# Optimization experiments

Hardware: AMD Instinct MI355X
Metric: run time of the kernel (lower is better)

Reference implementation:

```python
import jax, jax.numpy as jnp
import numpy as np

L, D, H, HK, DH, F, V, T, B = 8, 1024, 16, 4, 64, 2816, 32000, 1024, 2
G = H // HK
THETA = 10000.0
EPS = 1e-6
SCALE = DH ** -0.5


def _rope_tables(t, dh, theta):
    inv = 1.0 / theta ** (jnp.arange(0, dh, 2, dtype=jnp.float32) / dh)  # [dh/2]
    ang = jnp.arange(t, dtype=jnp.float32)[:, None] * inv[None, :]       # [T, dh/2]
    return jnp.cos(ang), jnp.sin(ang)


def _apply_rope(x, cos, sin):
    # x: [B, T, h, DH] -> rotate pairs (even, odd)
    xr = x.reshape(*x.shape[:-1], DH // 2, 2)
    x0, x1 = xr[..., 0], xr[..., 1]
    c = cos[None, :, None, :]
    s = sin[None, :, None, :]
    out = jnp.stack([x0 * c - x1 * s, x0 * s + x1 * c], axis=-1)
    return out.reshape(*x.shape)


def _rmsnorm(x, w):
    var = jnp.mean(x * x, axis=-1, keepdims=True)
    return x * jax.lax.rsqrt(var + EPS) * w


def setup_inputs() -> dict:
    key = jax.random.key(0)
    ks = jax.random.split(key, 10)
    s = 0.02
    return {
        "ids": jax.random.randint(ks[0], (B, T), 0, V),
        "emb": jax.random.normal(ks[1], (V, D), jnp.float32) * s,
        "qw": jax.random.normal(ks[2], (L, H * DH, D), jnp.float32) * s,
        "kw": jax.random.normal(ks[3], (L, HK * DH, D), jnp.float32) * s,
        "vw": jax.random.normal(ks[4], (L, HK * DH, D), jnp.float32) * s,
        "ow": jax.random.normal(ks[5], (L, D, D), jnp.float32) * s,
        "w1": jax.random.normal(ks[6], (L, F, D), jnp.float32) * s,
        "w2": jax.random.normal(ks[7], (L, D, F), jnp.float32) * s,
        "w3": jax.random.normal(ks[8], (L, F, D), jnp.float32) * s,
        "n1": jnp.ones((L, D), jnp.float32),
        "n2": jnp.ones((L, D), jnp.float32),
        "nf": jnp.ones((D,), jnp.float32),
    }


def _forward(ids, emb, qw, kw, vw, ow, w1, w2, w3, n1, n2, nf):
    cos, sin = _rope_tables(T, DH, THETA)
    causal = jnp.tril(jnp.ones((T, T), dtype=bool))  # [T, T]
    x = emb[ids]  # [B, T, D]
    for l in range(L):
        xn = _rmsnorm(x, n1[l])
        q = jnp.einsum("btd,ed->bte", xn, qw[l]).reshape(B, T, H, DH)
        k = jnp.einsum("btd,ed->bte", xn, kw[l]).reshape(B, T, HK, DH)
        v = jnp.einsum("btd,ed->bte", xn, vw[l]).reshape(B, T, HK, DH)
        q = _apply_rope(q, cos, sin)
        k = _apply_rope(k, cos, sin)
        # GQA: group query heads over shared kv heads
        qg = q.transpose(0, 2, 1, 3).reshape(B, HK, G, T, DH)
        kh = k.transpose(0, 2, 1, 3)  # [B, HK, T, DH]
        vh = v.transpose(0, 2, 1, 3)
        scores = jnp.einsum("bkgtd,bksd->bkgts", qg, kh) * SCALE
        scores = jnp.where(causal, scores, -jnp.inf)
        p = jax.nn.softmax(scores, axis=-1)
        out = jnp.einsum("bkgts,bksd->bkgtd", p, vh)
        out = out.reshape(B, H, T, DH).transpose(0, 2, 1, 3).reshape(B, T, D)
        x = x + jnp.einsum("btd,ed->bte", out, ow[l])
        xn2 = _rmsnorm(x, n2[l])
        h1 = jnp.einsum("btd,fd->btf", xn2, w1[l])
        h3 = jnp.einsum("btd,fd->btf", xn2, w3[l])
        x = x + jnp.einsum("btf,df->btd", jax.nn.silu(h1) * h3, w2[l])
    x = _rmsnorm(x, nf)
    logits = jnp.einsum("btd,vd->btv", x, emb)  # tied lm_head
    return logits


def reference(ids, emb, qw, kw, vw, ow, w1, w2, w3, n1, n2, nf):
    return _forward(ids, emb, qw, kw, vw, ow, w1, w2, w3, n1, n2, nf)
```

## Files before the change

kernel.cpp:

```cpp
#include <hip/hip_runtime.h>
#include <math.h>

#define L_ 8
#define D_ 1024
#define H_ 16
#define HK_ 4
#define DH_ 64
#define F_ 2816
#define V_ 32000
#define T_ 1024
#define B_ 2
#define M_ (B_*T_)
#define SCALE_ 0.125f

typedef unsigned short u16;
typedef unsigned int   u32;
typedef __attribute__((ext_vector_type(4))) float  f32x4;
typedef __attribute__((ext_vector_type(8))) short  bf16x8;
typedef __attribute__((ext_vector_type(4))) unsigned short u16x4;
typedef __attribute__((ext_vector_type(4))) unsigned int   u32x4;

__device__ __forceinline__ float bf2f(u16 h) {
    union { u32 u; float f; } v; v.u = ((u32)h) << 16; return v.f;
}
__device__ __forceinline__ u16 f2bf(float f) {
    union { float f; u32 u; } v; v.f = f;
    u32 r = v.u + 0x7fffu + ((v.u >> 16) & 1u);
    return (u16)(r >> 16);
}

__device__ __forceinline__ void gl_lds16(const void* g, void* l) {
    __builtin_amdgcn_global_load_lds(
        (const __attribute__((address_space(1))) unsigned int*)g,
        (__attribute__((address_space(3))) unsigned int*)l,
        16, 0, 0);
}

template<int BM, int EPI>
__global__ __launch_bounds__(256)
void gemm2_k(const u16* __restrict__ A, int K,
             const u16* __restrict__ W, int N,
             float* __restrict__ Of, u16* __restrict__ Ob)
{
    constexpr int FM = BM / 32;
    constexpr int FN = 4;
    constexpr int GM = M_ / BM;
    constexpr int IPA = BM / 64;
    __shared__ u16 sA[2 * BM * 32];
    __shared__ u16 sB[2 * 128 * 32];

    const int tid  = threadIdx.x;
    const int lane = tid & 63, wv = tid >> 6;
    const int wm = wv >> 1, wn = wv & 1;
    const int l15 = lane & 15, lhi = lane >> 4;
    const int m0 = wm * (BM / 2), n0 = wn * 64;

    const int nwg = gridDim.x;
    const int q8 = nwg >> 3, r8 = nwg & 7;
    const int xcd = blockIdx.x & 7, off8 = blockIdx.x >> 3;
    const int wgid = (xcd < r8 ? xcd * (q8 + 1) : r8 * (q8 + 1) + (xcd - r8) * q8) + off8;
    const int tM = wgid % GM, tN = wgid / GM;

    const int srow = lane >> 2;
    const int scol = (lane & 3) * 8;

    const u16* Abase = A + (size_t)(tM * BM) * K;
    const u16* Wbase = W + (size_t)(tN * 128) * K;

    f32x4 acc[FM][FN];
#pragma unroll
    for (int i = 0; i < FM; ++i)
#pragma unroll
        for (int j = 0; j < FN; ++j) acc[i][j] = f32x4{0.f, 0.f, 0.f, 0.f};

    auto stage = [&](int kt, int buf) {
        u16* sa = sA + buf * (BM * 32);
        u16* sb = sB + buf * (128 * 32);
#pragma unroll
        for (int i = 0; i < IPA; ++i) {
            int c = wv * IPA + i;
            gl_lds16(Abase + (size_t)(c * 16 + srow) * K + kt + scol, sa + c * 512);
        }
#pragma unroll
        for (int i = 0; i < 2; ++i) {
            int c = wv * 2 + i;
            gl_lds16(Wbase + (size_t)(c * 16 + srow) * K + kt + scol, sb + c * 512);
        }
    };

    const int nt = K >> 5;
    stage(0, 0);
    asm volatile("s_waitcnt vmcnt(0)" ::: "memory");
    __syncthreads();

    int cur = 0;
    for (int t = 0; t < nt; ++t) {
        if (t + 1 < nt) stage((t + 1) << 5, cur ^ 1);

        const u16* sa = sA + cur * (BM * 32);
        const u16* sb = sB + cur * (128 * 32);
        bf16x8 av[FM], bv[FN];
#pragma unroll
        for (int i = 0; i < FM; ++i)
            av[i] = *(const bf16x8*)&sa[(m0 + i * 16 + l15) * 32 + lhi * 8];
#pragma unroll
        for (int j = 0; j < FN; ++j)
            bv[j] = *(const bf16x8*)&sb[(n0 + j * 16 + l15) * 32 + lhi * 8];
#pragma unroll
        for (int i = 0; i < FM; ++i)
#pragma unroll
            for (int j = 0; j < FN; ++j)
                acc[i][j] = __builtin_amdgcn_mfma_f32_16x16x32_bf16(
                    av[i], bv[j], acc[i][j], 0, 0, 0);

        if (t + 1 < nt) {
            asm volatile("s_waitcnt vmcnt(0)" ::: "memory");
            __syncthreads();
            cur ^= 1;
        }
    }

#pragma unroll
    for (int i = 0; i < FM; ++i)
#pragma unroll
        for (int j = 0; j < FN; ++j) {
            size_t gm = (size_t)tM * BM + m0 + i * 16 + lhi * 4;
            size_t gn = (size_t)tN * 128 + n0 + j * 16 + l15;
#pragma unroll
            for (int r = 0; r < 4; ++r) {
                float v = acc[i][j][r];
                size_t idx = (gm + r) * (size_t)N + gn;
                if (EPI == 0)      Ob[idx] = f2bf(v);
                else if (EPI == 1) Of[idx] = v;
                else               Of[idx] += v;
            }
        }
}

__global__ __launch_bounds__(256)
void cvt_k(const float* __restrict__ src, u16* __restrict__ dst,
           unsigned long long sStride, unsigned long long dStride)
{
    int l = blockIdx.y;
    size_t i = ((size_t)blockIdx.x * 256 + threadIdx.x) * 4;
    f32x4 v = *(const f32x4*)(src + l * sStride + i);
    u16x4 o;
    o.x = f2bf(v.x); o.y = f2bf(v.y); o.z = f2bf(v.z); o.w = f2bf(v.w);
    *(u16x4*)(dst + l * dStride + i) = o;
}

template<int BM, int BN, int EPI, int NW>
__global__ __launch_bounds__(256)
void gemm_k(const u16* __restrict__ A, int K,
            const float* __restrict__ W0, const float* __restrict__ W1p,
            const float* __restrict__ W2p, int N0, int N1, int N,
            float* __restrict__ Of, u16* __restrict__ Ob)
{
    constexpr int FM = BM / 32;
    constexpr int FN = BN / 32;
    constexpr int LS = 40;
    __shared__ u16 sA[BM * LS];
    __shared__ u16 sB[BN * LS];

    const int tid  = threadIdx.x;
    const int lane = tid & 63, wv = tid >> 6;
    const int wm = wv >> 1, wn = wv & 1;
    const int l15 = lane & 15, lhi = lane >> 4;
    const int m0 = wm * (BM / 2), n0 = wn * (BN / 2);
    const int tM = blockIdx.y, tN = blockIdx.x;

    f32x4 acc[FM][FN];
#pragma unroll
    for (int i = 0; i < FM; ++i)
#pragma unroll
        for (int j = 0; j < FN; ++j) acc[i][j] = f32x4{0.f, 0.f, 0.f, 0.f};

    for (int kt = 0; kt < K; kt += 32) {
#pragma unroll
        for (int i = 0; i < BM / 64; ++i) {
            int cid = tid + i * 256;
            int row = cid >> 2, kc = cid & 3;
            const u16* src = A + (size_t)(tM * BM + row) * K + kt + kc * 8;
            *(u32x4*)&sA[row * LS + kc * 8] = *(const u32x4*)src;
        }
#pragma unroll
        for (int i = 0; i < BN / 32; ++i) {
            int cid = tid + i * 256;
            int row = cid >> 3, kc = cid & 7;
            int n = tN * BN + row;
            const float* wr;
            if (NW == 1)      wr = W0 + (size_t)n * K;
            else if (NW == 2) wr = (n < N0) ? (W0 + (size_t)n * K)
                                            : (W1p + (size_t)(n - N0) * K);
            else              wr = (n < N0) ? (W0 + (size_t)n * K)
                               : (n < N0 + N1) ? (W1p + (size_t)(n - N0) * K)
                                               : (W2p + (size_t)(n - N0 - N1) * K);
            f32x4 v = *(const f32x4*)(wr + kt + kc * 4);
            u16x4 o;
            o.x = f2bf(v.x); o.y = f2bf(v.y); o.z = f2bf(v.z); o.w = f2bf(v.w);
            *(u16x4*)&sB[row * LS + kc * 4] = o;
        }
        __syncthreads();

        bf16x8 av[FM], bv[FN];
#pragma unroll
        for (int i = 0; i < FM; ++i)
            av[i] = *(const bf16x8*)&sA[(m0 + i * 16 + l15) * LS + lhi * 8];
#pragma unroll
        for (int j = 0; j < FN; ++j)
            bv[j] = *(const bf16x8*)&sB[(n0 + j * 16 + l15) * LS + lhi * 8];
#pragma unroll
        for (int i = 0; i < FM; ++i)
#pragma unroll
            for (int j = 0; j < FN; ++j)
                acc[i][j] = __builtin_amdgcn_mfma_f32_16x16x32_bf16(
                    av[i], bv[j], acc[i][j], 0, 0, 0);
        __syncthreads();
    }

#pragma unroll
    for (int i = 0; i < FM; ++i)
#pragma unroll
        for (int j = 0; j < FN; ++j) {
            size_t gm = (size_t)tM * BM + m0 + i * 16 + lhi * 4;
            size_t gn = (size_t)tN * BN + n0 + j * 16 + l15;
#pragma unroll
            for (int r = 0; r < 4; ++r) {
                float v = acc[i][j][r];
                size_t idx = (gm + r) * (size_t)N + gn;
                if (EPI == 0)      Ob[idx] = f2bf(v);
                else if (EPI == 1) Of[idx] = v;
                else               Of[idx] += v;
            }
        }
}

__global__ __launch_bounds__(256)
void vtrans_k(const u16* __restrict__ qkv, u16* __restrict__ vt)
{
    int rr = blockIdx.x;
    int d = rr & 63, hk = (rr >> 6) & 3, b = rr >> 8;
    int t = threadIdx.x * 4;
    const u16* base = qkv + (size_t)(b * T_ + t) * 1536 + 1280 + hk * 64 + d;
    u16 a0 = base[0];
    u16 a1 = base[1536];
    u16 a2 = base[3072];
    u16 a3 = base[4608];
    u16x4 o; o.x = a0; o.y = a1; o.z = a2; o.w = a3;
    *(u16x4*)(vt + (size_t)rr * T_ + t) = o;
}

__global__ __launch_bounds__(256)
void attn2_k(const u16* __restrict__ qkv, const u16* __restrict__ vt,
             u16* __restrict__ attn)
{
    const int qt = blockIdx.x, h = blockIdx.y, b = blockIdx.z;
    const int hk = h >> 2;
    const int tid = threadIdx.x;
    const int lane = tid & 63, w = tid >> 6;
    const int l15 = lane & 15, lhi = lane >> 4;

    __shared__ u16 sK[128 * 64];
    __shared__ u16 sVT[64 * 128];
    __shared__ u16 sP[4][16 * 136];

    const int q0 = qt * 64;
    const u16* qptr = qkv + (size_t)(b * T_ + q0 + w * 16 + l15) * 1536 + h * 64 + lhi * 8;
    bf16x8 aq0 = *(const bf16x8*)qptr;
    bf16x8 aq1 = *(const bf16x8*)(qptr + 32);

    f32x4 accO[4];
#pragma unroll
    for (int d = 0; d < 4; ++d) accO[d] = f32x4{0.f, 0.f, 0.f, 0.f};
    float m_r[4] = {-1e30f, -1e30f, -1e30f, -1e30f};
    float l_r[4] = {0.f, 0.f, 0.f, 0.f};
    const int myq = q0 + w * 16 + lhi * 4;
    const int qmaxw = q0 + w * 16 + 15;
    u16* sPw = sP[w];

    const int ntiles = (qt + 2) >> 1;
    const u16* vtb = vt + (size_t)((b * HK_ + hk) * DH_) * T_;
    const int L = lane;

    for (int kt = 0; kt < ntiles; ++kt) {
        const int t0 = kt * 128;
#pragma unroll
        for (int i = 0; i < 4; ++i) {
            int c = w * 4 + i;
            int row = c * 8 + (L >> 3);
            int p = L & 7;
            const u16* src = qkv + (size_t)(b * T_ + t0 + row) * 1536 + 1024 + hk * 64
                             + ((p ^ (row & 7)) * 8);
            gl_lds16(src, sK + c * 512);
        }
#pragma unroll
        for (int i = 0; i < 4; ++i) {
            int c = w * 4 + i;
            int row = c * 4 + (L >> 4);
            int p = L & 15;
            const u16* src = vtb + (size_t)row * T_ + t0 + ((p ^ (row & 15)) * 8);
            gl_lds16(src, sVT + c * 512);
        }
        asm volatile("s_waitcnt vmcnt(0)" ::: "memory");
        __syncthreads();

        const bool lastt = (kt == ntiles - 1);

        f32x4 accS[8];
#pragma unroll
        for (int nf = 0; nf < 8; ++nf)
            accS[nf] = f32x4{-1e30f, -1e30f, -1e30f, -1e30f};
#pragma unroll
        for (int pk = 0; pk < 4; ++pk) {
            if (t0 + pk * 32 > qmaxw) continue;
            f32x4 s0 = f32x4{0.f, 0.f, 0.f, 0.f};
            f32x4 s1 = f32x4{0.f, 0.f, 0.f, 0.f};
#pragma unroll
            for (int kk = 0; kk < 2; ++kk) {
                bf16x8 aqs = kk ? aq1 : aq0;
                int r0 = (pk * 2) * 16 + l15;
                int r1 = (pk * 2 + 1) * 16 + l15;
                int ls = kk * 4 + lhi;
                bf16x8 b0 = *(const bf16x8*)&sK[r0 * 64 + ((ls ^ (r0 & 7)) * 8)];
                bf16x8 b1 = *(const bf16x8*)&sK[r1 * 64 + ((ls ^ (r1 & 7)) * 8)];
                s0 = __builtin_amdgcn_mfma_f32_16x16x32_bf16(aqs, b0, s0, 0, 0, 0);
                s1 = __builtin_amdgcn_mfma_f32_16x16x32_bf16(aqs, b1, s1, 0, 0, 0);
            }
#pragma unroll
            for (int r = 0; r < 4; ++r) {
                float v0 = s0[r] * SCALE_;
                float v1 = s1[r] * SCALE_;
                if (lastt) {
                    int kp0 = t0 + (pk * 2) * 16 + l15;
                    int kp1 = kp0 + 16;
                    if (kp0 > myq + r) v0 = -1e30f;
                    if (kp1 > myq + r) v1 = -1e30f;
                }
                accS[pk * 2][r] = v0;
                accS[pk * 2 + 1][r] = v1;
            }
        }

        float sc[4];
#pragma unroll
        for (int r = 0; r < 4; ++r) {
            float mx = accS[0][r];
#pragma unroll
            for (int nf = 1; nf < 8; ++nf) mx = fmaxf(mx, accS[nf][r]);
#pragma unroll
            for (int off = 1; off < 16; off <<= 1) mx = fmaxf(mx, __shfl_xor(mx, off));
            float mn = fmaxf(m_r[r], mx);
            sc[r] = expf(m_r[r] - mn);
            m_r[r] = mn;
        }
        float rs[4] = {0.f, 0.f, 0.f, 0.f};
#pragma unroll
        for (int pk = 0; pk < 4; ++pk) {
            if (t0 + pk * 32 > qmaxw) continue;
#pragma unroll
            for (int g = 0; g < 2; ++g) {
                int nf = pk * 2 + g;
#pragma unroll
                for (int r = 0; r < 4; ++r) {
                    float p = expf(accS[nf][r] - m_r[r]);
                    accS[nf][r] = p;
                    rs[r] += p;
                }
            }
        }
#pragma unroll
        for (int r = 0; r < 4; ++r) {
#pragma unroll
            for (int off = 1; off < 16; off <<= 1) rs[r] += __shfl_xor(rs[r], off);
            l_r[r] = l_r[r] * sc[r] + rs[r];
        }
#pragma unroll
        for (int d = 0; d < 4; ++d)
#pragma unroll
            for (int r = 0; r < 4; ++r) accO[d][r] *= sc[r];

#pragma unroll
        for (int pk = 0; pk < 4; ++pk) {
            if (t0 + pk * 32 > qmaxw) continue;
#pragma unroll
            for (int g = 0; g < 2; ++g) {
                int nf = pk * 2 + g;
#pragma unroll
                for (int r = 0; r < 4; ++r)
                    sPw[(lhi * 4 + r) * 136 + nf * 16 + l15] = f2bf(accS[nf][r]);
            }
        }

#pragma unroll
        for (int kk = 0; kk < 4; ++kk) {
            if (t0 + kk * 32 > qmaxw) continue;
            bf16x8 pas = *(const bf16x8*)&sPw[l15 * 136 + kk * 32 + lhi * 8];
#pragma unroll
            for (int nf = 0; nf < 4; ++nf) {
                int row = nf * 16 + l15;
                int ls = kk * 4 + lhi;
                bf16x8 bvv = *(const bf16x8*)&sVT[row * 128 + ((ls ^ (row & 15)) * 8)];
                accO[nf] = __builtin_amdgcn_mfma_f32_16x16x32_bf16(pas, bvv, accO[nf], 0, 0, 0);
            }
        }
        __syncthreads();
    }

#pragma unroll
    for (int d = 0; d < 4; ++d)
#pragma unroll
        for (int r = 0; r < 4; ++r) {
            int row = q0 + w * 16 + lhi * 4 + r;
            float o = accO[d][r] / l_r[r];
            attn[(size_t)(b * T_ + row) * 1024 + h * 64 + d * 16 + l15] = f2bf(o);
        }
}

__global__ __launch_bounds__(256)
void attn_k(const u16* __restrict__ qkv, u16* __restrict__ attn)
{
    const int qt = blockIdx.x, h = blockIdx.y, b = blockIdx.z;
    const int hk = h >> 2;
    const int tid = threadIdx.x;
    const int lane = tid & 63, w = tid >> 6;
    const int l15 = lane & 15, lhi = lane >> 4;
    __shared__ u16 sK[64 * 72];
    __shared__ u16 sVT[64 * 74];
    __shared__ u16 sP[4 * 16 * 72];

    const int q0 = qt * 64;
    const u16* qptr = qkv + (size_t)(b * T_ + q0 + w * 16 + l15) * 1536 + h * 64 + lhi * 8;
    bf16x8 aq0 = *(const bf16x8*)qptr;
    bf16x8 aq1 = *(const bf16x8*)(qptr + 32);

    f32x4 accO[4];
#pragma unroll
    for (int d = 0; d < 4; ++d) accO[d] = f32x4{0.f, 0.f, 0.f, 0.f};
    float m_r[4] = {-1e30f, -1e30f, -1e30f, -1e30f};
    float l_r[4] = {0.f, 0.f, 0.f, 0.f};
    const int myq = q0 + w * 16 + lhi * 4;
    u16* sPw = sP + w * 16 * 72;

    for (int kt = 0; kt <= qt; ++kt) {
#pragma unroll
        for (int i = 0; i < 2; ++i) {
            int cid = tid + i * 256;
            int r = cid >> 3, kc = cid & 7;
            const u16* src = qkv + (size_t)(b * T_ + kt * 64 + r) * 1536 + 1024 + hk * 64 + kc * 8;
            *(u32x4*)&sK[r * 72 + kc * 8] = *(const u32x4*)src;
        }
#pragma unroll
        for (int i = 0; i < 2; ++i) {
            int cid = tid + i * 256;
            int tt = cid >> 3, dc = cid & 7;
            const u16* src = qkv + (size_t)(b * T_ + kt * 64 + tt) * 1536 + 1280 + hk * 64 + dc * 8;
            bf16x8 vv = *(const bf16x8*)src;
#pragma unroll
            for (int j = 0; j < 8; ++j) sVT[(dc * 8 + j) * 74 + tt] = (u16)vv[j];
        }
        __syncthreads();

        f32x4 accS[4];
#pragma unroll
        for (int nf = 0; nf < 4; ++nf) accS[nf] = f32x4{0.f, 0.f, 0.f, 0.f};
#pragma unroll
        for (int s = 0; s < 2; ++s) {
            bf16x8 aqs = s ? aq1 : aq0;
#pragma unroll
            for (int nf = 0; nf < 4; ++nf) {
                bf16x8 bk = *(const bf16x8*)&sK[(nf * 16 + l15) * 72 + s * 32 + lhi * 8];
                accS[nf] = __builtin_amdgcn_mfma_f32_16x16x32_bf16(aqs, bk, accS[nf], 0, 0, 0);
            }
        }
#pragma unroll
        for (int nf = 0; nf < 4; ++nf)
#pragma unroll
            for (int r = 0; r < 4; ++r) {
                float v = accS[nf][r] * SCALE_;
                if (kt == qt) {
                    int kp = kt * 64 + nf * 16 + l15;
                    if (kp > myq + r) v = -1e30f;
                }
                accS[nf][r] = v;
            }
        float sc[4];
#pragma unroll
        for (int r = 0; r < 4; ++r) {
            float mx = fmaxf(fmaxf(accS[0][r], accS[1][r]), fmaxf(accS[2][r], accS[3][r]));
#pragma unroll
            for (int off = 1; off < 16; off <<= 1) mx = fmaxf(mx, __shfl_xor(mx, off));
            float mn = fmaxf(m_r[r], mx);
            sc[r] = expf(m_r[r] - mn);
            m_r[r] = mn;
        }
        float rs[4] = {0.f, 0.f, 0.f, 0.f};
#pragma unroll
        for (int nf = 0; nf < 4; ++nf)
#pragma unroll
            for (int r = 0; r < 4; ++r) {
                float p = expf(accS[nf][r] - m_r[r]);
                accS[nf][r] = p;
                rs[r] += p;
            }
#pragma unroll
        for (int r = 0; r < 4; ++r) {
#pragma unroll
            for (int off = 1; off < 16; off <<= 1) rs[r] += __shfl_xor(rs[r], off);
            l_r[r] = l_r[r] * sc[r] + rs[r];
        }
#pragma unroll
        for (int d = 0; d < 4; ++d)
#pragma unroll
            for (int r = 0; r < 4; ++r) accO[d][r] *= sc[r];

#pragma unroll
        for (int nf = 0; nf < 4; ++nf)
#pragma unroll
            for (int r = 0; r < 4; ++r)
                sPw[(lhi * 4 + r) * 72 + nf * 16 + l15] = f2bf(accS[nf][r]);
        bf16x8 pa0 = *(const bf16x8*)&sPw[l15 * 72 + lhi * 8];
        bf16x8 pa1 = *(const bf16x8*)&sPw[l15 * 72 + 32 + lhi * 8];
#pragma unroll
        for (int s = 0; s < 2; ++s) {
            bf16x8 pas = s ? pa1 : pa0;
#pragma unroll
            for (int d = 0; d < 4; ++d) {
                bf16x8 bvv = *(const bf16x8*)&sVT[(d * 16 + l15) * 74 + s * 32 + lhi * 8];
                accO[d] = __builtin_amdgcn_mfma_f32_16x16x32_bf16(pas, bvv, accO[d], 0, 0, 0);
            }
        }
        __syncthreads();
    }

#pragma unroll
    for (int d = 0; d < 4; ++d)
#pragma unroll
        for (int r = 0; r < 4; ++r) {
            int row = q0 + w * 16 + lhi * 4 + r;
            float o = accO[d][r] / l_r[r];
            attn[(size_t)(b * T_ + row) * 1024 + h * 64 + d * 16 + l15] = f2bf(o);
        }
}

__global__ __launch_bounds__(256)
void gather_k(const int* __restrict__ ids, const float* __restrict__ emb,
              float* __restrict__ x)
{
    int m = blockIdx.x, tid = threadIdx.x;
    int id = ids[m];
    *(f32x4*)(x + (size_t)m * D_ + tid * 4) =
        *(const f32x4*)(emb + (size_t)id * D_ + tid * 4);
}

__global__ __launch_bounds__(256)
void rmsnorm_k(const float* __restrict__ x, const float* __restrict__ g,
               u16* __restrict__ out)
{
    const int row = blockIdx.x, tid = threadIdx.x;
    const float* xr = x + (size_t)row * D_;
    f32x4 v = *(const f32x4*)(xr + tid * 4);
    float ss = v.x * v.x + v.y * v.y + v.z * v.z + v.w * v.w;
#pragma unroll
    for (int off = 32; off >= 1; off >>= 1) ss += __shfl_xor(ss, off);
    __shared__ float red[4];
    if ((tid & 63) == 0) red[tid >> 6] = ss;
    __syncthreads();
    float tot = red[0] + red[1] + red[2] + red[3];
    float rr = rsqrtf(tot * (1.0f / D_) + 1e-6f);
    f32x4 wv = *(const f32x4*)(g + tid * 4);
    u16x4 o;
    o.x = f2bf(v.x * rr * wv.x); o.y = f2bf(v.y * rr * wv.y);
    o.z = f2bf(v.z * rr * wv.z); o.w = f2bf(v.w * rr * wv.w);
    *(u16x4*)(out + (size_t)row * D_ + tid * 4) = o;
}

__global__ __launch_bounds__(256)
void rope_tab_k(float* __restrict__ tc, float* __restrict__ ts)
{
    int idx = blockIdx.x * 256 + threadIdx.x;
    int t = idx >> 5, j = idx & 31;
    float inv = powf(10000.0f, -(float)j * (1.0f / 32.0f));
    float ang = (float)t * inv;
    tc[idx] = cosf(ang);
    ts[idx] = sinf(ang);
}

__global__ __launch_bounds__(256)
void rope_k(u16* __restrict__ qkv, const float* __restrict__ tc,
            const float* __restrict__ ts)
{
    int idx = blockIdx.x * 256 + threadIdx.x;
    int m = idx / 160;
    int c = idx - m * 160;
    int t = m & (T_ - 1);
    int col = (c < 128) ? (c * 8) : (1024 + (c - 128) * 8);
    int j0 = (col & 63) >> 1;
    f32x4 cv = *(const f32x4*)(tc + t * 32 + j0);
    f32x4 sv = *(const f32x4*)(ts + t * 32 + j0);
    u16* p = qkv + (size_t)m * 1536 + col;
    bf16x8 v = *(const bf16x8*)p;
    bf16x8 o;
#pragma unroll
    for (int i = 0; i < 4; ++i) {
        float x0 = bf2f((u16)v[2 * i]), x1 = bf2f((u16)v[2 * i + 1]);
        o[2 * i]     = (short)f2bf(x0 * cv[i] - x1 * sv[i]);
        o[2 * i + 1] = (short)f2bf(x0 * sv[i] + x1 * cv[i]);
    }
    *(bf16x8*)p = o;
}

__global__ __launch_bounds__(256)
void silu_k(const u16* __restrict__ h13, u16* __restrict__ hh)
{
    int idx = blockIdx.x * 256 + threadIdx.x;
    int m = idx / 352;
    int c = idx - m * 352;
    const u16* h1p = h13 + (size_t)m * (2 * F_) + c * 8;
    bf16x8 a = *(const bf16x8*)h1p;
    bf16x8 b = *(const bf16x8*)(h1p + F_);
    bf16x8 o;
#pragma unroll
    for (int j = 0; j < 8; ++j) {
        float av = bf2f((u16)a[j]);
        float s = av / (1.0f + expf(-av));
        o[j] = (short)f2bf(s * bf2f((u16)b[j]));
    }
    *(bf16x8*)(hh + (size_t)m * F_ + c * 8) = o;
}

__global__ __launch_bounds__(256)
void silu_f32_k(const float* __restrict__ h13, u16* __restrict__ hh)
{
    int m = blockIdx.y;
    int f = blockIdx.x * 256 + threadIdx.x;
    float a = h13[(size_t)m * (2 * F_) + f];
    float c = h13[(size_t)m * (2 * F_) + F_ + f];
    float s = a / (1.0f + expf(-a));
    hh[(size_t)m * F_ + f] = f2bf(s * c);
}

__global__ __launch_bounds__(640)
void rope_slow_k(u16* __restrict__ qkv)
{
    int m = blockIdx.x;
    int c2 = threadIdx.x;
    int col = (c2 < 512) ? (c2 * 2) : (1024 + (c2 - 512) * 2);
    int d = col & 63;
    int t = m & (T_ - 1);
    float ang = (float)t * powf(10000.0f, -(float)d / 64.0f);
    float cs = cosf(ang), sn = sinf(ang);
    u16* p = qkv + (size_t)m * 1536 + col;
    float x0 = bf2f(p[0]), x1 = bf2f(p[1]);
    p[0] = f2bf(x0 * cs - x1 * sn);
    p[1] = f2bf(x0 * sn + x1 * cs);
}

extern "C" void kernel_launch(void* const* d_in, const int* in_sizes, int n_in,
                              void* d_out, int out_size, void* d_ws, size_t ws_size,
                              hipStream_t stream)
{
    const int*   ids = (const int*)d_in[0];
    const float* emb = (const float*)d_in[1];
    const float* qw  = (const float*)d_in[2];
    const float* kw  = (const float*)d_in[3];
    const float* vw  = (const float*)d_in[4];
    const float* ow  = (const float*)d_in[5];
    const float* w1  = (const float*)d_in[6];
    const float* w2  = (const float*)d_in[7];
    const float* w3  = (const float*)d_in[8];
    const float* n1  = (const float*)d_in[9];
    const float* n2  = (const float*)d_in[10];
    const float* nfw = (const float*)d_in[11];
    float* out = (float*)d_out;
    char*  ws  = (char*)d_ws;

    float* x    = (float*)(ws);
    u16*   xn   = (u16*)(ws + 8388608ULL);
    u16*   qkvb = (u16*)(ws + 12582912ULL);
    u16*   attnb= (u16*)(ws + 18874368ULL);
    u16*   h13  = (u16*)(ws + 23068672ULL);
    u16*   hh   = (u16*)(ws + 46137344ULL);
    float* ropec= (float*)(ws + 57671680ULL);
    float* ropes= (float*)(ws + 57802752ULL);
    u16*   embb = (u16*)(ws + 57933824ULL);
    u16*   wqkv = (u16*)(ws + 123469824ULL);
    u16*   wob  = (u16*)(ws + 148635648ULL);
    u16*   w13b = (u16*)(ws + 165412864ULL);
    u16*   w2b  = (u16*)(ws + 257687552ULL);
    u16*   vtb  = (u16*)(ws + 303824896ULL);
    const unsigned long long NEED = 304873472ULL;

    if (ws_size >= NEED) {
        cvt_k<<<dim3(32000, 1), 256, 0, stream>>>(emb, embb, 0, 0);
        cvt_k<<<dim3(1024, L_), 256, 0, stream>>>(qw, wqkv,            1048576ULL, 1572864ULL);
        cvt_k<<<dim3(256,  L_), 256, 0, stream>>>(kw, wqkv + 1048576,  262144ULL,  1572864ULL);
        cvt_k<<<dim3(256,  L_), 256, 0, stream>>>(vw, wqkv + 1310720,  262144ULL,  1572864ULL);
        cvt_k<<<dim3(1024, L_), 256, 0, stream>>>(ow, wob,             1048576ULL, 1048576ULL);
        cvt_k<<<dim3(2816, L_), 256, 0, stream>>>(w1, w13b,            2883584ULL, 5767168ULL);
        cvt_k<<<dim3(2816, L_), 256, 0, stream>>>(w3, w13b + 2883584,  2883584ULL, 5767168ULL);
        cvt_k<<<dim3(2816, L_), 256, 0, stream>>>(w2, w2b,             2883584ULL, 2883584ULL);
        rope_tab_k<<<T_ * 32 / 256, 256, 0, stream>>>(ropec, ropes);

        gather_k<<<M_, 256, 0, stream>>>(ids, emb, x);

        for (int l = 0; l < L_; ++l) {
            rmsnorm_k<<<M_, 256, 0, stream>>>(x, n1 + l * D_, xn);
            gemm2_k<64, 0><<<32 * 12, 256, 0, stream>>>(
                xn, D_, wqkv + (size_t)l * 1572864, 1536, nullptr, qkvb);
            rope_k<<<M_ * 160 / 256, 256, 0, stream>>>(qkvb, ropec, ropes);
            vtrans_k<<<B_ * HK_ * DH_, 256, 0, stream>>>(qkvb, vtb);
            attn2_k<<<dim3(T_ / 64, H_, B_), 256, 0, stream>>>(qkvb, vtb, attnb);
            gemm2_k<64, 2><<<32 * 8, 256, 0, stream>>>(
                attnb, D_, wob + (size_t)l * 1048576, 1024, x, nullptr);
            rmsnorm_k<<<M_, 256, 0, stream>>>(x, n2 + l * D_, xn);
            gemm2_k<128, 0><<<16 * 44, 256, 0, stream>>>(
                xn, D_, w13b + (size_t)l * 5767168, 2 * F_, nullptr, h13);
            silu_k<<<M_ * 352 / 256, 256, 0, stream>>>(h13, hh);
            gemm2_k<64, 2><<<32 * 8, 256, 0, stream>>>(
                hh, F_, w2b + (size_t)l * 2883584, 1024, x, nullptr);
        }

        rmsnorm_k<<<M_, 256, 0, stream>>>(x, nfw, xn);
        gemm2_k<128, 1><<<16 * 250, 256, 0, stream>>>(
            xn, D_, embb, V_, out, nullptr);
        return;
    }

    float* h13f = (float*)(ws + 23068672ULL);
    u16*   hhf  = (u16*)(ws + 69206016ULL);
    gather_k<<<M_, 256, 0, stream>>>(ids, emb, x);

    for (int l = 0; l < L_; ++l) {
        rmsnorm_k<<<M_, 256, 0, stream>>>(x, n1 + l * D_, xn);
        gemm_k<128, 64, 0, 3><<<dim3(24, 16), 256, 0, stream>>>(
            xn, D_,
            qw + (size_t)l * H_ * DH_ * D_,
            kw + (size_t)l * HK_ * DH_ * D_,
            vw + (size_t)l * HK_ * DH_ * D_,
            1024, 256, 1536, nullptr, qkvb);
        rope_slow_k<<<M_, 640, 0, stream>>>(qkvb);
        attn_k<<<dim3(T_ / 64, H_, B_), 256, 0, stream>>>(qkvb, attnb);
        gemm_k<128, 64, 2, 1><<<dim3(16, 16), 256, 0, stream>>>(
            attnb, D_, ow + (size_t)l * D_ * D_, nullptr, nullptr,
            0, 0, D_, x, nullptr);
        rmsnorm_k<<<M_, 256, 0, stream>>>(x, n2 + l * D_, xn);
        gemm_k<128, 128, 1, 2><<<dim3(44, 16), 256, 0, stream>>>(
            xn, D_, w1 + (size_t)l * F_ * D_, w3 + (size_t)l * F_ * D_, nullptr,
            F_, 0, 2 * F_, h13f, nullptr);
        silu_f32_k<<<dim3(11, M_), 256, 0, stream>>>(h13f, hhf);
        gemm_k<128, 64, 2, 1><<<dim3(16, 16), 256, 0, stream>>>(
            hhf, F_, w2 + (size_t)l * D_ * F_, nullptr, nullptr,
            0, 0, D_, x, nullptr);
    }

    rmsnorm_k<<<M_, 256, 0, stream>>>(x, nfw, xn);
    gemm_k<128, 128, 1, 1><<<dim3(250, 16), 256, 0, stream>>>(
        xn, D_, emb, nullptr, nullptr, 0, 0, V_, out, nullptr);
}
```

Measured before the change: 1.987 ms.

## Triple-buffer GEMM pipeline and fuse RoPE and SwiGLU into GEMM epilogues

Replaces the double-buffered GEMM with a three-stage global-to-LDS pipeline that waits on partial vmcnt counts, so loads for two tiles ahead stay in flight. RoPE is applied inside the QKV GEMM epilogue using lane shuffles to fetch the paired element. W1 and W3 rows are interleaved so that SiLU(h1)*h3 can be computed in the gate/up GEMM epilogue, which drops the separate rope and silu kernels and the intermediate h13 buffer. The costs are more LDS per block and lane-shuffle work in the epilogue, and correctness depends on the interleaved pairing lining up with the MFMA output layout.

```diff
diff --git a/kernel.cpp b/kernel.cpp
--- a/kernel.cpp
+++ b/kernel.cpp
@@ -36,18 +36,28 @@
         16, 0, 0);
 }
 
+template<int N> __device__ __forceinline__ void vm_wait() {
+    if constexpr (N == 0) asm volatile("s_waitcnt vmcnt(0)" ::: "memory");
+    else if constexpr (N == 3) asm volatile("s_waitcnt vmcnt(3)" ::: "memory");
+    else if constexpr (N == 4) asm volatile("s_waitcnt vmcnt(4)" ::: "memory");
+    else if constexpr (N == 6) asm volatile("s_waitcnt vmcnt(6)" ::: "memory");
+    else if constexpr (N == 8) asm volatile("s_waitcnt vmcnt(8)" ::: "memory");
+}
+
 template<int BM, int EPI>
 __global__ __launch_bounds__(256)
-void gemm2_k(const u16* __restrict__ A, int K,
+void gemm3_k(const u16* __restrict__ A, int K,
              const u16* __restrict__ W, int N,
-             float* __restrict__ Of, u16* __restrict__ Ob)
+             float* __restrict__ Of, u16* __restrict__ Ob,
+             const float* __restrict__ tc, const float* __restrict__ ts)
 {
     constexpr int FM = BM / 32;
     constexpr int FN = 4;
     constexpr int GM = M_ / BM;
     constexpr int IPA = BM / 64;
-    __shared__ u16 sA[2 * BM * 32];
-    __shared__ u16 sB[2 * 128 * 32];
+    constexpr int LPT = IPA + 2;
+    __shared__ u16 sA[3 * BM * 32];
+    __shared__ u16 sB[3 * 128 * 32];
 
     const int tid  = threadIdx.x;
     const int lane = tid & 63, wv = tid >> 6;
@@ -73,7 +83,8 @@
 #pragma unroll
         for (int j = 0; j < FN; ++j) acc[i][j] = f32x4{0.f, 0.f, 0.f, 0.f};
 
-    auto stage = [&](int kt, int buf) {
+    auto stage = [&](int t, int buf) {
+        const int kt = t << 5;
         u16* sa = sA + buf * (BM * 32);
         u16* sb = sB + buf * (128 * 32);
 #pragma unroll
@@ -90,15 +101,16 @@
 
     const int nt = K >> 5;
     stage(0, 0);
-    asm volatile("s_waitcnt vmcnt(0)" ::: "memory");
-    __syncthreads();
-
-    int cur = 0;
+    stage(1, 1);
+
     for (int t = 0; t < nt; ++t) {
-        if (t + 1 < nt) stage((t + 1) << 5, cur ^ 1);
-
-        const u16* sa = sA + cur * (BM * 32);
-        const u16* sb = sB + cur * (128 * 32);
+        if (t + 2 < nt) { stage(t + 2, (t + 2) % 3); vm_wait<2 * LPT>(); }
+        else if (t + 1 < nt) vm_wait<LPT>();
+        else vm_wait<0>();
+        __builtin_amdgcn_s_barrier();
+
+        const u16* sa = sA + (t % 3) * (BM * 32);
+        const u16* sb = sB + (t % 3) * (128 * 32);
         bf16x8 av[FM], bv[FN];
 #pragma unroll
         for (int i = 0; i < FM; ++i)
@@ -114,9 +126,8 @@
                     av[i], bv[j], acc[i][j], 0, 0, 0);
 
         if (t + 1 < nt) {
-            asm volatile("s_waitcnt vmcnt(0)" ::: "memory");
-            __syncthreads();
-            cur ^= 1;
+            asm volatile("s_waitcnt lgkmcnt(0)" ::: "memory");
+            __builtin_amdgcn_s_barrier();
         }
     }
 
@@ -130,9 +141,31 @@
             for (int r = 0; r < 4; ++r) {
                 float v = acc[i][j][r];
                 size_t idx = (gm + r) * (size_t)N + gn;
-                if (EPI == 0)      Ob[idx] = f2bf(v);
-                else if (EPI == 1) Of[idx] = v;
-                else               Of[idx] += v;
+                if (EPI == 0) {
+                    Ob[idx] = f2bf(v);
+                } else if (EPI == 1) {
+                    Of[idx] = v;
+                } else if (EPI == 2) {
+                    Of[idx] += v;
+                } else if (EPI == 3) {
+                    float b = __shfl_xor(v, 1);
+                    if ((lane & 1) == 0) {
+                        float s = v / (1.0f + expf(-v));
+                        Ob[(gm + r) * (size_t)F_ + (gn >> 1)] = f2bf(s * b);
+                    }
+                } else {
+                    float b = __shfl_xor(v, 1);
+                    if ((int)gn < 1280) {
+                        int dd = (int)gn & 63;
+                        int jj = dd >> 1;
+                        int tt = (int)(gm + r) & (T_ - 1);
+                        float c = tc[tt * 32 + jj], s = ts[tt * 32 + jj];
+                        float ro = ((dd & 1) == 0) ? (v * c - b * s) : (b * s + v * c);
+                        Ob[idx] = f2bf(ro);
+                    } else {
+                        Ob[idx] = f2bf(v);
+                    }
+                }
             }
         }
 }
@@ -147,6 +180,18 @@
     u16x4 o;
     o.x = f2bf(v.x); o.y = f2bf(v.y); o.z = f2bf(v.z); o.w = f2bf(v.w);
     *(u16x4*)(dst + l * dStride + i) = o;
+}
+
+__global__ __launch_bounds__(256)
+void cvt_il_k(const float* __restrict__ src, u16* __restrict__ dst,
+              unsigned long long sStride, unsigned long long dStride, int off)
+{
+    int f = blockIdx.x, l = blockIdx.y;
+    int i = threadIdx.x * 4;
+    f32x4 v = *(const f32x4*)(src + l * sStride + (size_t)f * D_ + i);
+    u16x4 o;
+    o.x = f2bf(v.x); o.y = f2bf(v.y); o.z = f2bf(v.z); o.w = f2bf(v.w);
+    *(u16x4*)(dst + l * dStride + (size_t)(2 * f + off) * D_ + i) = o;
 }
 
 template<int BM, int BN, int EPI, int NW>
@@ -586,49 +631,6 @@
 }
 
 __global__ __launch_bounds__(256)
-void rope_k(u16* __restrict__ qkv, const float* __restrict__ tc,
-            const float* __restrict__ ts)
-{
-    int idx = blockIdx.x * 256 + threadIdx.x;
-    int m = idx / 160;
-    int c = idx - m * 160;
-    int t = m & (T_ - 1);
-    int col = (c < 128) ? (c * 8) : (1024 + (c - 128) * 8);
-    int j0 = (col & 63) >> 1;
-    f32x4 cv = *(const f32x4*)(tc + t * 32 + j0);
-    f32x4 sv = *(const f32x4*)(ts + t * 32 + j0);
-    u16* p = qkv + (size_t)m * 1536 + col;
-    bf16x8 v = *(const bf16x8*)p;
-    bf16x8 o;
-#pragma unroll
-    for (int i = 0; i < 4; ++i) {
-        float x0 = bf2f((u16)v[2 * i]), x1 = bf2f((u16)v[2 * i + 1]);
-        o[2 * i]     = (short)f2bf(x0 * cv[i] - x1 * sv[i]);
-        o[2 * i + 1] = (short)f2bf(x0 * sv[i] + x1 * cv[i]);
-    }
-    *(bf16x8*)p = o;
-}
-
-__global__ __launch_bounds__(256)
-void silu_k(const u16* __restrict__ h13, u16* __restrict__ hh)
-{
-    int idx = blockIdx.x * 256 + threadIdx.x;
-    int m = idx / 352;
-    int c = idx - m * 352;
-    const u16* h1p = h13 + (size_t)m * (2 * F_) + c * 8;
-    bf16x8 a = *(const bf16x8*)h1p;
-    bf16x8 b = *(const bf16x8*)(h1p + F_);
-    bf16x8 o;
-#pragma unroll
-    for (int j = 0; j < 8; ++j) {
-        float av = bf2f((u16)a[j]);
-        float s = av / (1.0f + expf(-av));
-        o[j] = (short)f2bf(s * bf2f((u16)b[j]));
-    }
-    *(bf16x8*)(hh + (size_t)m * F_ + c * 8) = o;
-}
-
-__global__ __launch_bounds__(256)
 void silu_f32_k(const float* __restrict__ h13, u16* __restrict__ hh)
 {
     int m = blockIdx.y;
@@ -678,7 +680,6 @@
     u16*   xn   = (u16*)(ws + 8388608ULL);
     u16*   qkvb = (u16*)(ws + 12582912ULL);
     u16*   attnb= (u16*)(ws + 18874368ULL);
-    u16*   h13  = (u16*)(ws + 23068672ULL);
     u16*   hh   = (u16*)(ws + 46137344ULL);
     float* ropec= (float*)(ws + 57671680ULL);
     float* ropes= (float*)(ws + 57802752ULL);
@@ -696,8 +697,8 @@
         cvt_k<<<dim3(256,  L_), 256, 0, stream>>>(kw, wqkv + 1048576,  262144ULL,  1572864ULL);
         cvt_k<<<dim3(256,  L_), 256, 0, stream>>>(vw, wqkv + 1310720,  262144ULL,  1572864ULL);
         cvt_k<<<dim3(1024, L_), 256, 0, stream>>>(ow, wob,             1048576ULL, 1048576ULL);
-        cvt_k<<<dim3(2816, L_), 256, 0, stream>>>(w1, w13b,            2883584ULL, 5767168ULL);
-        cvt_k<<<dim3(2816, L_), 256, 0, stream>>>(w3, w13b + 2883584,  2883584ULL, 5767168ULL);
+        cvt_il_k<<<dim3(2816, L_), 256, 0, stream>>>(w1, w13b, 2883584ULL, 5767168ULL, 0);
+        cvt_il_k<<<dim3(2816, L_), 256, 0, stream>>>(w3, w13b, 2883584ULL, 5767168ULL, 1);
         cvt_k<<<dim3(2816, L_), 256, 0, stream>>>(w2, w2b,             2883584ULL, 2883584ULL);
         rope_tab_k<<<T_ * 32 / 256, 256, 0, stream>>>(ropec, ropes);
 
@@ -705,24 +706,22 @@
 
         for (int l = 0; l < L_; ++l) {
             rmsnorm_k<<<M_, 256, 0, stream>>>(x, n1 + l * D_, xn);
-            gemm2_k<64, 0><<<32 * 12, 256, 0, stream>>>(
-                xn, D_, wqkv + (size_t)l * 1572864, 1536, nullptr, qkvb);
-            rope_k<<<M_ * 160 / 256, 256, 0, stream>>>(qkvb, ropec, ropes);
+            gemm3_k<64, 4><<<32 * 12, 256, 0, stream>>>(
+                xn, D_, wqkv + (size_t)l * 1572864, 1536, nullptr, qkvb, ropec, ropes);
             vtrans_k<<<B_ * HK_ * DH_, 256, 0, stream>>>(qkvb, vtb);
             attn2_k<<<dim3(T_ / 64, H_, B_), 256, 0, stream>>>(qkvb, vtb, attnb);
-            gemm2_k<64, 2><<<32 * 8, 256, 0, stream>>>(
-                attnb, D_, wob + (size_t)l * 1048576, 1024, x, nullptr);
+            gemm3_k<64, 2><<<32 * 8, 256, 0, stream>>>(
+                attnb, D_, wob + (size_t)l * 1048576, 1024, x, nullptr, nullptr, nullptr);
             rmsnorm_k<<<M_, 256, 0, stream>>>(x, n2 + l * D_, xn);
-            gemm2_k<128, 0><<<16 * 44, 256, 0, stream>>>(
-                xn, D_, w13b + (size_t)l * 5767168, 2 * F_, nullptr, h13);
-            silu_k<<<M_ * 352 / 256, 256, 0, stream>>>(h13, hh);
-            gemm2_k<64, 2><<<32 * 8, 256, 0, stream>>>(
-                hh, F_, w2b + (size_t)l * 2883584, 1024, x, nullptr);
+            gemm3_k<128, 3><<<16 * 44, 256, 0, stream>>>(
+                xn, D_, w13b + (size_t)l * 5767168, 5632, nullptr, hh, nullptr, nullptr);
+            gemm3_k<64, 2><<<32 * 8, 256, 0, stream>>>(
+                hh, F_, w2b + (size_t)l * 2883584, 1024, x, nullptr, nullptr, nullptr);
         }
 
         rmsnorm_k<<<M_, 256, 0, stream>>>(x, nfw, xn);
-        gemm2_k<128, 1><<<16 * 250, 256, 0, stream>>>(
-            xn, D_, embb, V_, out, nullptr);
+        gemm3_k<128, 1><<<16 * 250, 256, 0, stream>>>(
+            xn, D_, embb, V_, out, nullptr, nullptr, nullptr);
         return;
     }
 
```

Result: no change. 2.025 ms (+1.9%).
